# Optimization experiments

Hardware: AMD Instinct MI355X
Metric: run time of the kernel (lower is better)

The kernel has to match this reference:

```python
import jax, jax.numpy as jnp
import numpy as np


def _make_dplr_hippo(N):
    # Standard HiPPO-LegS -> NPLR -> DPLR construction (Annotated S4).
    p = np.sqrt(1.0 + 2.0 * np.arange(N))
    A = p[:, None] * p[None, :]
    A = np.tril(A) - np.diag(np.arange(N))
    A = -A
    P = np.sqrt(np.arange(N) + 0.5)
    B = np.sqrt(2.0 * np.arange(N) + 1.0)
    # Normal part S = A + P P^T is skew-symmetric + const*I
    S = A + P[:, None] * P[None, :]
    Lambda_real = np.mean(np.diagonal(S)) * np.ones(N)  # = -0.5
    Lambda_imag, V = np.linalg.eigh(S * -1j)            # S*-1j is Hermitian
    Lambda = Lambda_real + 1j * Lambda_imag
    Pc = V.conj().T @ P
    Bc = V.conj().T @ B
    return Lambda, Pc, Bc


N_STATE = 64
SEQ_LEN = 16384
BATCH = 1024


def setup_inputs() -> dict:
    key = jax.random.key(0)
    kx, kcr, kci = jax.random.split(key, 3)
    Lambda, P, B = _make_dplr_hippo(N_STATE)
    scale = 0.5 ** 0.5
    return {
        "x": jax.random.normal(kx, (BATCH, SEQ_LEN), dtype=jnp.float32),
        "Lambda_real": jnp.asarray(Lambda.real, dtype=jnp.float32),
        "Lambda_imag": jnp.asarray(Lambda.imag, dtype=jnp.float32),
        "P_real": jnp.asarray(P.real, dtype=jnp.float32),
        "P_imag": jnp.asarray(P.imag, dtype=jnp.float32),
        "B_real": jnp.asarray(B.real, dtype=jnp.float32),
        "B_imag": jnp.asarray(B.imag, dtype=jnp.float32),
        "C_real": jax.random.normal(kcr, (N_STATE,), dtype=jnp.float32) * scale,
        "C_imag": jax.random.normal(kci, (N_STATE,), dtype=jnp.float32) * scale,
        "step_size": jnp.asarray(0.01, dtype=jnp.float32),
    }


def _s4_fourier_kernel(Lambda, P, Q, B, C, step, L):
    # Evaluate the DPLR SSM generating function at the L roots of unity
    # via 4 Cauchy dot products (the classic S4 bottleneck).
    k = jnp.arange(L, dtype=jnp.float32)
    Omega = jnp.exp(-2j * jnp.pi * k / L)                 # [L] complex64
    g = (2.0 / step) * (1.0 - Omega) / (1.0 + Omega)      # [L]
    c = 2.0 / (1.0 + Omega)                               # [L]
    inv = 1.0 / (g[:, None] - Lambda[None, :])            # [L, N] Cauchy denominators
    a0 = jnp.conj(C)
    a1 = jnp.conj(Q)
    k00 = inv @ (a0 * B)   # [L]
    k01 = inv @ (a0 * P)
    k10 = inv @ (a1 * B)
    k11 = inv @ (a1 * P)
    return c * (k00 - k01 * (1.0 / (1.0 + k11)) * k10)    # [L]


def reference(x, Lambda_real, Lambda_imag, P_real, P_imag, B_real, B_imag,
              C_real, C_imag, step_size):
    L = x.shape[-1]
    Lambda = Lambda_real + 1j * Lambda_imag
    P = P_real + 1j * P_imag
    B = B_real + 1j * B_imag
    C_tilde = C_real + 1j * C_imag
    # Original computes the kernel under torch.no_grad().
    kernel = _s4_fourier_kernel(Lambda, P, P, B, C_tilde, step_size, L)  # [L]
    fft_u = jnp.fft.fft(x, n=L)              # [batch, L] complex64
    y = jnp.fft.ifft(kernel * fft_u, n=L)    # circular conv in freq domain
    return y.real
```

## Files before the change

### kernel.cpp

```cpp
#include <hip/hip_runtime.h>
#include <math.h>

#define LFFT 16384
#define NTHREADS 1024
#define LDS_PITCH 17

#define LDS_FENCE() asm volatile("s_waitcnt lgkmcnt(0)" ::: "memory")

__device__ __forceinline__ float2 cadd(float2 a, float2 b){ return make_float2(a.x+b.x, a.y+b.y); }
__device__ __forceinline__ float2 csub(float2 a, float2 b){ return make_float2(a.x-b.x, a.y-b.y); }
__device__ __forceinline__ float2 cmul(float2 a, float2 b){ return make_float2(a.x*b.x - a.y*b.y, a.x*b.y + a.y*b.x); }

template<int S> __device__ __forceinline__ float2 mul_is(float2 a) {
    return make_float2(-(float)S * a.y, (float)S * a.x);
}

template<int S> __device__ __forceinline__ void dft4_t(float2& a0, float2& a1, float2& a2, float2& a3) {
    float2 t0 = cadd(a0, a2);
    float2 t1 = csub(a0, a2);
    float2 t2 = cadd(a1, a3);
    float2 t3 = csub(a1, a3);
    a0 = cadd(t0, t2);
    a2 = csub(t0, t2);
    const float s = (float)S;
    a1 = make_float2(t1.x - s * t3.y, t1.y + s * t3.x);
    a3 = make_float2(t1.x + s * t3.y, t1.y - s * t3.x);
}

#define C16A 0.92387953251128675613f
#define C16B 0.70710678118654752440f
#define C16C 0.38268343236508977173f

template<int S> __device__ __forceinline__ void dft16_t(float2 r[16]) {
    const float s = (float)S;
    const float2 w1 = make_float2( C16A, s * C16C);
    const float2 w2 = make_float2( C16B, s * C16B);
    const float2 w3 = make_float2( C16C, s * C16A);
    const float2 w6 = make_float2(-C16B, s * C16B);
    const float2 w9 = make_float2(-C16A, -s * C16C);
    float2 g[4][4];
    #pragma unroll
    for (int b = 0; b < 4; ++b) {
        float2 a0 = r[b], a1 = r[b+4], a2 = r[b+8], a3 = r[b+12];
        dft4_t<S>(a0, a1, a2, a3);
        g[b][0] = a0; g[b][1] = a1; g[b][2] = a2; g[b][3] = a3;
    }
    g[1][1] = cmul(g[1][1], w1);  g[1][2] = cmul(g[1][2], w2);  g[1][3] = cmul(g[1][3], w3);
    g[2][1] = cmul(g[2][1], w2);  g[2][2] = mul_is<S>(g[2][2]); g[2][3] = cmul(g[2][3], w6);
    g[3][1] = cmul(g[3][1], w3);  g[3][2] = cmul(g[3][2], w6);  g[3][3] = cmul(g[3][3], w9);
    #pragma unroll
    for (int ka = 0; ka < 4; ++ka) {
        float2 a0 = g[0][ka], a1 = g[1][ka], a2 = g[2][ka], a3 = g[3][ka];
        dft4_t<S>(a0, a1, a2, a3);
        r[ka] = a0; r[ka+4] = a1; r[ka+8] = a2; r[ka+12] = a3;
    }
}

__device__ __forceinline__ void twiddle15(float2 r[16], float2 w) {
    float2 w2 = cmul(w, w);
    float2 we = w2;
    float2 wo = cmul(w, w2);
    r[1] = cmul(r[1], w);
    r[2] = cmul(r[2], we);
    r[3] = cmul(r[3], wo);
    #pragma unroll
    for (int j = 2; j <= 7; ++j) {
        we = cmul(we, w2);  r[2*j]   = cmul(r[2*j],   we);
        wo = cmul(wo, w2);  r[2*j+1] = cmul(r[2*j+1], wo);
    }
}

__global__ void s4_tables(const float* __restrict__ Lr, const float* __restrict__ Li,
                          const float* __restrict__ Pr, const float* __restrict__ Pi,
                          const float* __restrict__ Br, const float* __restrict__ Bi,
                          const float* __restrict__ Cr, const float* __restrict__ Ci,
                          const float* __restrict__ step_ptr,
                          float2* __restrict__ Kperm, float2* __restrict__ twid)
{
    __shared__ double part[256][8];
    const int tid = threadIdx.x;
    const int T = blockIdx.x * 256 + tid;
    const int p = T >> 3, e = (T >> 2) & 1, q = T & 3;

    int t16 = p >> 4, j = p & 15;
    int m = (t16 >> 6) + 16 * ((t16 >> 2) & 15)
          + 256 * (4 * (t16 & 3) + (j >> 2)) + 4096 * (j & 3);
    int idx = e ? ((LFFT - m) & (LFFT - 1)) : m;

    const double step = (double)step_ptr[0];
    const double tn = tan((M_PI / (double)LFFT) * (double)idx);
    const double gi = (2.0 / step) * tn;

    double k00r=0,k00i=0,k01r=0,k01i=0,k10r=0,k10i=0,k11r=0,k11i=0;
    const int n0 = 16 * q;
    for (int n = n0; n < n0 + 16; ++n) {
        double dr = -(double)Lr[n];
        double di = gi - (double)Li[n];
        double id2 = 1.0 / (dr*dr + di*di);
        double vr =  dr * id2;
        double vi = -di * id2;
        double a0r = (double)Cr[n], a0i = -(double)Ci[n];
        double a1r = (double)Pr[n], a1i = -(double)Pi[n];
        double br  = (double)Br[n], bi  = (double)Bi[n];
        double pr  = (double)Pr[n], pi  = (double)Pi[n];
        double e00r = a0r*br - a0i*bi, e00i = a0r*bi + a0i*br;
        double e01r = a0r*pr - a0i*pi, e01i = a0r*pi + a0i*pr;
        double e10r = a1r*br - a1i*bi, e10i = a1r*bi + a1i*br;
        double e11r = a1r*pr - a1i*pi, e11i = a1r*pi + a1i*pr;
        k00r += vr*e00r - vi*e00i;  k00i += vr*e00i + vi*e00r;
        k01r += vr*e01r - vi*e01i;  k01i += vr*e01i + vi*e01r;
        k10r += vr*e10r - vi*e10i;  k10i += vr*e10i + vi*e10r;
        k11r += vr*e11r - vi*e11i;  k11i += vr*e11i + vi*e11r;
    }
    part[tid][0] = k00r;  part[tid][1] = k00i;
    part[tid][2] = k01r;  part[tid][3] = k01i;
    part[tid][4] = k10r;  part[tid][5] = k10i;
    part[tid][6] = k11r;  part[tid][7] = k11i;

    if ((T & 7) == 1) {
        double tth = (-2.0 * M_PI / (double)LFFT) * (double)p;
        double si, co;
        sincos(tth, &si, &co);
        twid[p] = make_float2((float)co, (float)si);
    }
    __syncthreads();

    if ((T & 7) == 0) {
        double Kr[2], Ki[2];
        #pragma unroll
        for (int ev = 0; ev < 2; ++ev) {
            double s[8] = {0,0,0,0,0,0,0,0};
            #pragma unroll
            for (int qq = 0; qq < 4; ++qq) {
                const double* pp = part[tid + 4*ev + qq];
                #pragma unroll
                for (int z = 0; z < 8; ++z) s[z] += pp[z];
            }
            double rr = 1.0 + s[6], ri = s[7];
            double ir2 = 1.0 / (rr*rr + ri*ri);
            double qr0 = s[2]*s[4] - s[3]*s[5];
            double qi0 = s[2]*s[5] + s[3]*s[4];
            double qr = (qr0*rr + qi0*ri) * ir2;
            double qi = (qi0*rr - qr0*ri) * ir2;
            double sr = s[0] - qr, sim = s[1] - qi;
            double tc = (ev == 0) ? tn : -tn;
            Kr[ev] = sr - tc * sim;
            Ki[ev] = sim + tc * sr;
        }
        const float sc = 0.5f / (float)LFFT;
        Kperm[p] = make_float2(sc * (float)(Kr[0] + Kr[1]),
                               sc * (float)(Ki[0] - Ki[1]));
    }
}

__global__ __launch_bounds__(NTHREADS, 4) void fft_conv(
    const float* __restrict__ x, float* __restrict__ y,
    const float2* __restrict__ twid, const float2* __restrict__ kperm)
{
    __shared__ float2 lds[NTHREADS * LDS_PITCH];
    const int t    = threadIdx.x;
    const int lane = t & 63;
    const int w    = t >> 6;
    const int l2   = t & 3;
    const int h    = (t >> 2) & 15;
    const size_t rowbase = (size_t)blockIdx.x * 2u * LFFT;
    const float* x0 = x + rowbase;
    const float* x1 = x0 + LFFT;

    float2 r[16];

    #pragma unroll
    for (int a = 0; a < 16; ++a)
        r[a] = make_float2(x0[t + NTHREADS*a], x1[t + NTHREADS*a]);

    dft16_t<-1>(r);
    twiddle15(r, twid[t]);

    #pragma unroll
    for (int k = 0; k < 16; ++k)
        lds[(k*64 + lane) * LDS_PITCH + w] = r[k];
    __syncthreads();
    #pragma unroll
    for (int a = 0; a < 16; ++a)
        r[a] = lds[t * LDS_PITCH + a];
    LDS_FENCE();

    dft16_t<-1>(r);
    twiddle15(r, twid[16 * lane]);

    #pragma unroll
    for (int k = 0; k < 16; ++k)
        lds[(w*64 + 4*k + l2) * LDS_PITCH + h] = r[k];
    LDS_FENCE();
    #pragma unroll
    for (int a = 0; a < 16; ++a)
        r[a] = lds[t * LDS_PITCH + a];
    LDS_FENCE();

    dft16_t<-1>(r);
    twiddle15(r, twid[256 * l2]);

    #pragma unroll
    for (int k = 0; k < 16; ++k)
        lds[((t & ~3) + (k >> 2)) * LDS_PITCH + 4*(k & 3) + l2] = r[k];
    LDS_FENCE();
    #pragma unroll
    for (int j = 0; j < 16; ++j)
        r[j] = lds[t * LDS_PITCH + j];
    LDS_FENCE();

    #pragma unroll
    for (int q = 0; q < 4; ++q)
        dft4_t<-1>(r[4*q], r[4*q+1], r[4*q+2], r[4*q+3]);

    {
        const float4* kp4 = (const float4*)(kperm + t * 16);
        #pragma unroll
        for (int c = 0; c < 2; ++c) {
            float4 kv[4];
            #pragma unroll
            for (int i = 0; i < 4; ++i) kv[i] = kp4[4*c + i];
            #pragma unroll
            for (int i = 0; i < 4; ++i) {
                r[8*c + 2*i]     = cmul(r[8*c + 2*i],     make_float2(kv[i].x, kv[i].y));
                r[8*c + 2*i + 1] = cmul(r[8*c + 2*i + 1], make_float2(kv[i].z, kv[i].w));
            }
        }
    }

    #pragma unroll
    for (int q = 0; q < 4; ++q)
        dft4_t<1>(r[4*q], r[4*q+1], r[4*q+2], r[4*q+3]);

    #pragma unroll
    for (int j = 0; j < 16; ++j)
        lds[((t & ~3) + (j & 3)) * LDS_PITCH + ((4*l2 + (j >> 2)) ^ h)] = r[j];
    LDS_FENCE();
    #pragma unroll
    for (int k = 0; k < 16; ++k)
        r[k] = lds[t * LDS_PITCH + (k ^ h)];
    LDS_FENCE();

    { float2 ww = twid[256 * l2]; twiddle15(r, make_float2(ww.x, -ww.y)); }
    dft16_t<1>(r);

    #pragma unroll
    for (int a = 0; a < 16; ++a)
        lds[(w*64 + l2 + 4*a) * LDS_PITCH + h] = r[a];
    LDS_FENCE();
    #pragma unroll
    for (int k = 0; k < 16; ++k)
        r[k] = lds[t * LDS_PITCH + k];

    { float2 ww = twid[16 * lane]; twiddle15(r, make_float2(ww.x, -ww.y)); }
    dft16_t<1>(r);

    __syncthreads();
    #pragma unroll
    for (int a = 0; a < 16; ++a)
        lds[(lane + 64*a) * LDS_PITCH + w] = r[a];
    __syncthreads();
    #pragma unroll
    for (int k = 0; k < 16; ++k)
        r[k] = lds[t * LDS_PITCH + k];

    { float2 ww = twid[t]; twiddle15(r, make_float2(ww.x, -ww.y)); }
    dft16_t<1>(r);

    float* y0 = y + rowbase;
    float* y1 = y0 + LFFT;
    #pragma unroll
    for (int a = 0; a < 16; ++a) {
        y0[t + NTHREADS*a] = r[a].x;
        y1[t + NTHREADS*a] = r[a].y;
    }
}

extern "C" void kernel_launch(void* const* d_in, const int* in_sizes, int n_in,
                              void* d_out, int out_size, void* d_ws, size_t ws_size,
                              hipStream_t stream)
{
    const float* x  = (const float*)d_in[0];
    const float* Lr = (const float*)d_in[1];
    const float* Li = (const float*)d_in[2];
    const float* Pr = (const float*)d_in[3];
    const float* Pi = (const float*)d_in[4];
    const float* Br = (const float*)d_in[5];
    const float* Bi = (const float*)d_in[6];
    const float* Cr = (const float*)d_in[7];
    const float* Ci = (const float*)d_in[8];
    const float* st = (const float*)d_in[9];

    const int rows = in_sizes[0] / LFFT;

    float2* twid  = (float2*)d_ws;
    float2* Kperm = twid + LFFT;

    s4_tables<<<(8 * LFFT) / 256, 256, 0, stream>>>(Lr, Li, Pr, Pi, Br, Bi,
                                                    Cr, Ci, st, Kperm, twid);
    fft_conv<<<rows / 2, NTHREADS, 0, stream>>>(x, (float*)d_out, twid, Kperm);
}
```

Before: 67.12 us.

## Fuse kernel table build and FFT convolution into one cooperative kernel

Merges the Cauchy-kernel/twiddle table computation and the FFT convolution into a single cooperatively launched kernel, separated by a grid-wide sync. The table partial sums reuse the FFT shared-memory buffer. The grid is halved so each block handles two row pairs in a loop. The aim is to remove the second kernel launch and its gap. In exchange it adds grid-sync cost, and it packs the double-precision table work into fewer, larger blocks, so half the blocks sit idle during that phase.

```diff
diff --git a/kernel.cpp b/kernel.cpp
--- a/kernel.cpp
+++ b/kernel.cpp
@@ -1,5 +1,8 @@
 #include <hip/hip_runtime.h>
+#include <hip/hip_cooperative_groups.h>
 #include <math.h>
+
+namespace cg = cooperative_groups;
 
 #define LFFT 16384
 #define NTHREADS 1024
@@ -70,209 +73,222 @@
     }
 }
 
-__global__ void s4_tables(const float* __restrict__ Lr, const float* __restrict__ Li,
-                          const float* __restrict__ Pr, const float* __restrict__ Pi,
-                          const float* __restrict__ Br, const float* __restrict__ Bi,
-                          const float* __restrict__ Cr, const float* __restrict__ Ci,
-                          const float* __restrict__ step_ptr,
-                          float2* __restrict__ Kperm, float2* __restrict__ twid)
-{
-    __shared__ double part[256][8];
-    const int tid = threadIdx.x;
-    const int T = blockIdx.x * 256 + tid;
-    const int p = T >> 3, e = (T >> 2) & 1, q = T & 3;
-
-    int t16 = p >> 4, j = p & 15;
-    int m = (t16 >> 6) + 16 * ((t16 >> 2) & 15)
-          + 256 * (4 * (t16 & 3) + (j >> 2)) + 4096 * (j & 3);
-    int idx = e ? ((LFFT - m) & (LFFT - 1)) : m;
-
-    const double step = (double)step_ptr[0];
-    const double tn = tan((M_PI / (double)LFFT) * (double)idx);
-    const double gi = (2.0 / step) * tn;
-
-    double k00r=0,k00i=0,k01r=0,k01i=0,k10r=0,k10i=0,k11r=0,k11i=0;
-    const int n0 = 16 * q;
-    for (int n = n0; n < n0 + 16; ++n) {
-        double dr = -(double)Lr[n];
-        double di = gi - (double)Li[n];
-        double id2 = 1.0 / (dr*dr + di*di);
-        double vr =  dr * id2;
-        double vi = -di * id2;
-        double a0r = (double)Cr[n], a0i = -(double)Ci[n];
-        double a1r = (double)Pr[n], a1i = -(double)Pi[n];
-        double br  = (double)Br[n], bi  = (double)Bi[n];
-        double pr  = (double)Pr[n], pi  = (double)Pi[n];
-        double e00r = a0r*br - a0i*bi, e00i = a0r*bi + a0i*br;
-        double e01r = a0r*pr - a0i*pi, e01i = a0r*pi + a0i*pr;
-        double e10r = a1r*br - a1i*bi, e10i = a1r*bi + a1i*br;
-        double e11r = a1r*pr - a1i*pi, e11i = a1r*pi + a1i*pr;
-        k00r += vr*e00r - vi*e00i;  k00i += vr*e00i + vi*e00r;
-        k01r += vr*e01r - vi*e01i;  k01i += vr*e01i + vi*e01r;
-        k10r += vr*e10r - vi*e10i;  k10i += vr*e10i + vi*e10r;
-        k11r += vr*e11r - vi*e11i;  k11i += vr*e11i + vi*e11r;
-    }
-    part[tid][0] = k00r;  part[tid][1] = k00i;
-    part[tid][2] = k01r;  part[tid][3] = k01i;
-    part[tid][4] = k10r;  part[tid][5] = k10i;
-    part[tid][6] = k11r;  part[tid][7] = k11i;
-
-    if ((T & 7) == 1) {
-        double tth = (-2.0 * M_PI / (double)LFFT) * (double)p;
-        double si, co;
-        sincos(tth, &si, &co);
-        twid[p] = make_float2((float)co, (float)si);
-    }
-    __syncthreads();
-
-    if ((T & 7) == 0) {
-        double Kr[2], Ki[2];
-        #pragma unroll
-        for (int ev = 0; ev < 2; ++ev) {
-            double s[8] = {0,0,0,0,0,0,0,0};
-            #pragma unroll
-            for (int qq = 0; qq < 4; ++qq) {
-                const double* pp = part[tid + 4*ev + qq];
-                #pragma unroll
-                for (int z = 0; z < 8; ++z) s[z] += pp[z];
-            }
-            double rr = 1.0 + s[6], ri = s[7];
-            double ir2 = 1.0 / (rr*rr + ri*ri);
-            double qr0 = s[2]*s[4] - s[3]*s[5];
-            double qi0 = s[2]*s[5] + s[3]*s[4];
-            double qr = (qr0*rr + qi0*ri) * ir2;
-            double qi = (qi0*rr - qr0*ri) * ir2;
-            double sr = s[0] - qr, sim = s[1] - qi;
-            double tc = (ev == 0) ? tn : -tn;
-            Kr[ev] = sr - tc * sim;
-            Ki[ev] = sim + tc * sr;
-        }
-        const float sc = 0.5f / (float)LFFT;
-        Kperm[p] = make_float2(sc * (float)(Kr[0] + Kr[1]),
-                               sc * (float)(Ki[0] - Ki[1]));
-    }
-}
-
-__global__ __launch_bounds__(NTHREADS, 4) void fft_conv(
+__global__ __launch_bounds__(NTHREADS, 4) void s4_all(
     const float* __restrict__ x, float* __restrict__ y,
-    const float2* __restrict__ twid, const float2* __restrict__ kperm)
+    const float* __restrict__ Lr, const float* __restrict__ Li,
+    const float* __restrict__ Pr, const float* __restrict__ Pi,
+    const float* __restrict__ Br, const float* __restrict__ Bi,
+    const float* __restrict__ Cr, const float* __restrict__ Ci,
+    const float* __restrict__ step_ptr,
+    float2* __restrict__ Kperm, float2* __restrict__ twid)
 {
     __shared__ float2 lds[NTHREADS * LDS_PITCH];
-    const int t    = threadIdx.x;
+    const int t = threadIdx.x;
+
+    {
+        double* part = reinterpret_cast<double*>(lds);
+        const int T = blockIdx.x * NTHREADS + t;
+        const bool active = (T < 8 * LFFT);
+        double tn = 0.0;
+        int p = 0;
+        if (active) {
+            p = T >> 3;
+            const int e = (T >> 2) & 1, q = T & 3;
+            int t16 = p >> 4, j = p & 15;
+            int m = (t16 >> 6) + 16 * ((t16 >> 2) & 15)
+                  + 256 * (4 * (t16 & 3) + (j >> 2)) + 4096 * (j & 3);
+            int idx = e ? ((LFFT - m) & (LFFT - 1)) : m;
+
+            const double step = (double)step_ptr[0];
+            tn = tan((M_PI / (double)LFFT) * (double)idx);
+            const double gi = (2.0 / step) * tn;
+
+            double k00r=0,k00i=0,k01r=0,k01i=0,k10r=0,k10i=0,k11r=0,k11i=0;
+            const int n0 = 16 * q;
+            for (int n = n0; n < n0 + 16; ++n) {
+                double dr = -(double)Lr[n];
+                double di = gi - (double)Li[n];
+                double id2 = 1.0 / (dr*dr + di*di);
+                double vr =  dr * id2;
+                double vi = -di * id2;
+                double a0r = (double)Cr[n], a0i = -(double)Ci[n];
+                double a1r = (double)Pr[n], a1i = -(double)Pi[n];
+                double br  = (double)Br[n], bi  = (double)Bi[n];
+                double pr  = (double)Pr[n], pi  = (double)Pi[n];
+                double e00r = a0r*br - a0i*bi, e00i = a0r*bi + a0i*br;
+                double e01r = a0r*pr - a0i*pi, e01i = a0r*pi + a0i*pr;
+                double e10r = a1r*br - a1i*bi, e10i = a1r*bi + a1i*br;
+                double e11r = a1r*pr - a1i*pi, e11i = a1r*pi + a1i*pr;
+                k00r += vr*e00r - vi*e00i;  k00i += vr*e00i + vi*e00r;
+                k01r += vr*e01r - vi*e01i;  k01i += vr*e01i + vi*e01r;
+                k10r += vr*e10r - vi*e10i;  k10i += vr*e10i + vi*e10r;
+                k11r += vr*e11r - vi*e11i;  k11i += vr*e11i + vi*e11r;
+            }
+            double* pp = part + t * 8;
+            pp[0] = k00r;  pp[1] = k00i;
+            pp[2] = k01r;  pp[3] = k01i;
+            pp[4] = k10r;  pp[5] = k10i;
+            pp[6] = k11r;  pp[7] = k11i;
+
+            if ((T & 7) == 1) {
+                double tth = (-2.0 * M_PI / (double)LFFT) * (double)p;
+                double si, co;
+                sincos(tth, &si, &co);
+                twid[p] = make_float2((float)co, (float)si);
+            }
+        }
+        __syncthreads();
+        if (active && (T & 7) == 0) {
+            double Kr[2], Ki[2];
+            #pragma unroll
+            for (int ev = 0; ev < 2; ++ev) {
+                double s[8] = {0,0,0,0,0,0,0,0};
+                #pragma unroll
+                for (int qq = 0; qq < 4; ++qq) {
+                    const double* pp = part + (t + 4*ev + qq) * 8;
+                    #pragma unroll
+                    for (int z = 0; z < 8; ++z) s[z] += pp[z];
+                }
+                double rr = 1.0 + s[6], ri = s[7];
+                double ir2 = 1.0 / (rr*rr + ri*ri);
+                double qr0 = s[2]*s[4] - s[3]*s[5];
+                double qi0 = s[2]*s[5] + s[3]*s[4];
+                double qr = (qr0*rr + qi0*ri) * ir2;
+                double qi = (qi0*rr - qr0*ri) * ir2;
+                double sr = s[0] - qr, sim = s[1] - qi;
+                double tc = (ev == 0) ? tn : -tn;
+                Kr[ev] = sr - tc * sim;
+                Ki[ev] = sim + tc * sr;
+            }
+            const float sc = 0.5f / (float)LFFT;
+            Kperm[p] = make_float2(sc * (float)(Kr[0] + Kr[1]),
+                                   sc * (float)(Ki[0] - Ki[1]));
+        }
+    }
+
+    __threadfence();
+    cg::this_grid().sync();
+
     const int lane = t & 63;
     const int w    = t >> 6;
     const int l2   = t & 3;
     const int h    = (t >> 2) & 15;
-    const size_t rowbase = (size_t)blockIdx.x * 2u * LFFT;
-    const float* x0 = x + rowbase;
-    const float* x1 = x0 + LFFT;
-
-    float2 r[16];
-
-    #pragma unroll
-    for (int a = 0; a < 16; ++a)
-        r[a] = make_float2(x0[t + NTHREADS*a], x1[t + NTHREADS*a]);
-
-    dft16_t<-1>(r);
-    twiddle15(r, twid[t]);
-
-    #pragma unroll
-    for (int k = 0; k < 16; ++k)
-        lds[(k*64 + lane) * LDS_PITCH + w] = r[k];
-    __syncthreads();
-    #pragma unroll
-    for (int a = 0; a < 16; ++a)
-        r[a] = lds[t * LDS_PITCH + a];
-    LDS_FENCE();
-
-    dft16_t<-1>(r);
-    twiddle15(r, twid[16 * lane]);
-
-    #pragma unroll
-    for (int k = 0; k < 16; ++k)
-        lds[(w*64 + 4*k + l2) * LDS_PITCH + h] = r[k];
-    LDS_FENCE();
-    #pragma unroll
-    for (int a = 0; a < 16; ++a)
-        r[a] = lds[t * LDS_PITCH + a];
-    LDS_FENCE();
-
-    dft16_t<-1>(r);
-    twiddle15(r, twid[256 * l2]);
-
-    #pragma unroll
-    for (int k = 0; k < 16; ++k)
-        lds[((t & ~3) + (k >> 2)) * LDS_PITCH + 4*(k & 3) + l2] = r[k];
-    LDS_FENCE();
-    #pragma unroll
-    for (int j = 0; j < 16; ++j)
-        r[j] = lds[t * LDS_PITCH + j];
-    LDS_FENCE();
-
-    #pragma unroll
-    for (int q = 0; q < 4; ++q)
-        dft4_t<-1>(r[4*q], r[4*q+1], r[4*q+2], r[4*q+3]);
-
-    {
-        const float4* kp4 = (const float4*)(kperm + t * 16);
-        #pragma unroll
-        for (int c = 0; c < 2; ++c) {
-            float4 kv[4];
+    const float2* kperm = Kperm;
+
+    for (int it = 0; it < 2; ++it) {
+        __syncthreads();
+
+        const size_t rowbase = ((size_t)blockIdx.x + (size_t)gridDim.x * it) * 2u * LFFT;
+        const float* x0 = x + rowbase;
+        const float* x1 = x0 + LFFT;
+
+        float2 r[16];
+
+        #pragma unroll
+        for (int a = 0; a < 16; ++a)
+            r[a] = make_float2(x0[t + NTHREADS*a], x1[t + NTHREADS*a]);
+
+        dft16_t<-1>(r);
+        twiddle15(r, twid[t]);
+
+        #pragma unroll
+        for (int k = 0; k < 16; ++k)
+            lds[(k*64 + lane) * LDS_PITCH + w] = r[k];
+        __syncthreads();
+        #pragma unroll
+        for (int a = 0; a < 16; ++a)
+            r[a] = lds[t * LDS_PITCH + a];
+        LDS_FENCE();
+
+        dft16_t<-1>(r);
+        twiddle15(r, twid[16 * lane]);
+
+        #pragma unroll
+        for (int k = 0; k < 16; ++k)
+            lds[(w*64 + 4*k + l2) * LDS_PITCH + h] = r[k];
+        LDS_FENCE();
+        #pragma unroll
+        for (int a = 0; a < 16; ++a)
+            r[a] = lds[t * LDS_PITCH + a];
+        LDS_FENCE();
+
+        dft16_t<-1>(r);
+        twiddle15(r, twid[256 * l2]);
+
+        #pragma unroll
+        for (int k = 0; k < 16; ++k)
+            lds[((t & ~3) + (k >> 2)) * LDS_PITCH + 4*(k & 3) + l2] = r[k];
+        LDS_FENCE();
+        #pragma unroll
+        for (int j = 0; j < 16; ++j)
+            r[j] = lds[t * LDS_PITCH + j];
+        LDS_FENCE();
+
+        #pragma unroll
+        for (int q = 0; q < 4; ++q)
+            dft4_t<-1>(r[4*q], r[4*q+1], r[4*q+2], r[4*q+3]);
+
+        {
+            const float4* kp4 = (const float4*)(kperm + t * 16);
             #pragma unroll
-            for (int i = 0; i < 4; ++i) kv[i] = kp4[4*c + i];
-            #pragma unroll
-            for (int i = 0; i < 4; ++i) {
-                r[8*c + 2*i]     = cmul(r[8*c + 2*i],     make_float2(kv[i].x, kv[i].y));
-                r[8*c + 2*i + 1] = cmul(r[8*c + 2*i + 1], make_float2(kv[i].z, kv[i].w));
+            for (int c = 0; c < 2; ++c) {
+                float4 kv[4];
+                #pragma unroll
+                for (int i = 0; i < 4; ++i) kv[i] = kp4[4*c + i];
+                #pragma unroll
+                for (int i = 0; i < 4; ++i) {
+                    r[8*c + 2*i]     = cmul(r[8*c + 2*i],     make_float2(kv[i].x, kv[i].y));
+                    r[8*c + 2*i + 1] = cmul(r[8*c + 2*i + 1], make_float2(kv[i].z, kv[i].w));
+                }
             }
         }
-    }
-
-    #pragma unroll
-    for (int q = 0; q < 4; ++q)
-        dft4_t<1>(r[4*q], r[4*q+1], r[4*q+2], r[4*q+3]);
-
-    #pragma unroll
-    for (int j = 0; j < 16; ++j)
-        lds[((t & ~3) + (j & 3)) * LDS_PITCH + ((4*l2 + (j >> 2)) ^ h)] = r[j];
-    LDS_FENCE();
-    #pragma unroll
-    for (int k = 0; k < 16; ++k)
-        r[k] = lds[t * LDS_PITCH + (k ^ h)];
-    LDS_FENCE();
-
-    { float2 ww = twid[256 * l2]; twiddle15(r, make_float2(ww.x, -ww.y)); }
-    dft16_t<1>(r);
-
-    #pragma unroll
-    for (int a = 0; a < 16; ++a)
-        lds[(w*64 + l2 + 4*a) * LDS_PITCH + h] = r[a];
-    LDS_FENCE();
-    #pragma unroll
-    for (int k = 0; k < 16; ++k)
-        r[k] = lds[t * LDS_PITCH + k];
-
-    { float2 ww = twid[16 * lane]; twiddle15(r, make_float2(ww.x, -ww.y)); }
-    dft16_t<1>(r);
-
-    __syncthreads();
-    #pragma unroll
-    for (int a = 0; a < 16; ++a)
-        lds[(lane + 64*a) * LDS_PITCH + w] = r[a];
-    __syncthreads();
-    #pragma unroll
-    for (int k = 0; k < 16; ++k)
-        r[k] = lds[t * LDS_PITCH + k];
-
-    { float2 ww = twid[t]; twiddle15(r, make_float2(ww.x, -ww.y)); }
-    dft16_t<1>(r);
-
-    float* y0 = y + rowbase;
-    float* y1 = y0 + LFFT;
-    #pragma unroll
-    for (int a = 0; a < 16; ++a) {
-        y0[t + NTHREADS*a] = r[a].x;
-        y1[t + NTHREADS*a] = r[a].y;
+
+        #pragma unroll
+        for (int q = 0; q < 4; ++q)
+            dft4_t<1>(r[4*q], r[4*q+1], r[4*q+2], r[4*q+3]);
+
+        #pragma unroll
+        for (int j = 0; j < 16; ++j)
+            lds[((t & ~3) + (j & 3)) * LDS_PITCH + ((4*l2 + (j >> 2)) ^ h)] = r[j];
+        LDS_FENCE();
+        #pragma unroll
+        for (int k = 0; k < 16; ++k)
+            r[k] = lds[t * LDS_PITCH + (k ^ h)];
+        LDS_FENCE();
+
+        { float2 ww = twid[256 * l2]; twiddle15(r, make_float2(ww.x, -ww.y)); }
+        dft16_t<1>(r);
+
+        #pragma unroll
+        for (int a = 0; a < 16; ++a)
+            lds[(w*64 + l2 + 4*a) * LDS_PITCH + h] = r[a];
+        LDS_FENCE();
+        #pragma unroll
+        for (int k = 0; k < 16; ++k)
+            r[k] = lds[t * LDS_PITCH + k];
+
+        { float2 ww = twid[16 * lane]; twiddle15(r, make_float2(ww.x, -ww.y)); }
+        dft16_t<1>(r);
+
+        __syncthreads();
+        #pragma unroll
+        for (int a = 0; a < 16; ++a)
+            lds[(lane + 64*a) * LDS_PITCH + w] = r[a];
+        __syncthreads();
+        #pragma unroll
+        for (int k = 0; k < 16; ++k)
+            r[k] = lds[t * LDS_PITCH + k];
+
+        { float2 ww = twid[t]; twiddle15(r, make_float2(ww.x, -ww.y)); }
+        dft16_t<1>(r);
+
+        float* y0 = y + rowbase;
+        float* y1 = y0 + LFFT;
+        #pragma unroll
+        for (int a = 0; a < 16; ++a) {
+            y0[t + NTHREADS*a] = r[a].x;
+            y1[t + NTHREADS*a] = r[a].y;
+        }
     }
 }
 
@@ -290,13 +306,18 @@
     const float* Cr = (const float*)d_in[7];
     const float* Ci = (const float*)d_in[8];
     const float* st = (const float*)d_in[9];
-
-    const int rows = in_sizes[0] / LFFT;
+    float* y = (float*)d_out;
+
+    const int rows   = in_sizes[0] / LFFT;
+    const int blocks = rows / 4;
 
     float2* twid  = (float2*)d_ws;
     float2* Kperm = twid + LFFT;
 
-    s4_tables<<<(8 * LFFT) / 256, 256, 0, stream>>>(Lr, Li, Pr, Pi, Br, Bi,
-                                                    Cr, Ci, st, Kperm, twid);
-    fft_conv<<<rows / 2, NTHREADS, 0, stream>>>(x, (float*)d_out, twid, Kperm);
-}
+    void* args[] = { (void*)&x, (void*)&y, (void*)&Lr, (void*)&Li,
+                     (void*)&Pr, (void*)&Pi, (void*)&Br, (void*)&Bi,
+                     (void*)&Cr, (void*)&Ci, (void*)&st,
+                     (void*)&Kperm, (void*)&twid };
+    hipLaunchCooperativeKernel((void*)s4_all, dim3(blocks), dim3(NTHREADS),
+                               args, 0, stream);
+}
```

Result: slower. 182.6 us (+172.0%).
